# Kernel optimization log

Hardware: AMD Instinct MI355X
Metric: run time of the kernel (lower is better)

## Reference

```python
import jax, jax.numpy as jnp
import numpy as np

N_CLASS = 29   # len('SE?abcdefghijklmnopqrstuvwxyz')
N_HIDDEN = 128


def _rnn(x, h0, Wih, Whh, bih, bhh):
    """PyTorch nn.RNN (tanh, 1 layer, batch_first) semantics.
    x: [B,T,I], h0: [B,H]. Returns (outputs [B,T,H], h_T [B,H]).
    h_t = tanh(x_t @ Wih^T + bih + h_{t-1} @ Whh^T + bhh)
    """
    # Precompute input projection for all timesteps (batched GEMM).
    xp = jnp.einsum('bti,hi->bth', x, Wih) + (bih + bhh)  # [B,T,H]

    def step(h, xt):  # xt: [B,H]
        h_new = jnp.tanh(xt + h @ Whh.T)
        return h_new, h_new

    hT, hs = jax.lax.scan(step, h0, jnp.swapaxes(xp, 0, 1))  # scan over T
    return jnp.swapaxes(hs, 0, 1), hT


def setup_inputs() -> dict:
    key = jax.random.key(0)
    ks = jax.random.split(key, 12)
    B, T = 2048, 256
    s = 1.0 / np.sqrt(N_HIDDEN)  # PyTorch RNN/Linear init scale
    inp = {
        'encoder_input': jax.random.normal(ks[0], (B, T, N_CLASS), jnp.float32),
        'encoder_hidden': jnp.zeros((1, B, N_HIDDEN), jnp.float32),
        'decoder_input': jax.random.normal(ks[1], (B, T, N_CLASS), jnp.float32),
        'enc_Wih': jax.random.uniform(ks[2], (N_HIDDEN, N_CLASS), jnp.float32, -s, s),
        'enc_Whh': jax.random.uniform(ks[3], (N_HIDDEN, N_HIDDEN), jnp.float32, -s, s),
        'enc_bih': jax.random.uniform(ks[4], (N_HIDDEN,), jnp.float32, -s, s),
        'enc_bhh': jax.random.uniform(ks[5], (N_HIDDEN,), jnp.float32, -s, s),
        'dec_Wih': jax.random.uniform(ks[6], (N_HIDDEN, N_CLASS), jnp.float32, -s, s),
        'dec_Whh': jax.random.uniform(ks[7], (N_HIDDEN, N_HIDDEN), jnp.float32, -s, s),
        'dec_bih': jax.random.uniform(ks[8], (N_HIDDEN,), jnp.float32, -s, s),
        'dec_bhh': jax.random.uniform(ks[9], (N_HIDDEN,), jnp.float32, -s, s),
        'fc_W': jax.random.uniform(ks[10], (N_CLASS, N_HIDDEN), jnp.float32, -s, s),
        'fc_b': jax.random.uniform(ks[11], (N_CLASS,), jnp.float32, -s, s),
    }
    return inp


def reference(encoder_input, encoder_hidden, decoder_input,
              enc_Wih, enc_Whh, enc_bih, enc_bhh,
              dec_Wih, dec_Whh, dec_bih, dec_bhh,
              fc_W, fc_b):
    h0 = encoder_hidden[0]                                   # [B,H]
    _, h_t = _rnn(encoder_input, h0, enc_Wih, enc_Whh, enc_bih, enc_bhh)
    dec_out, _ = _rnn(decoder_input, h_t, dec_Wih, dec_Whh, dec_bih, dec_bhh)  # [B,T,H]
    return jnp.einsum('bth,ch->btc', dec_out, fc_W) + fc_b   # [B,T,n_class]
```

## Files before the change

kernel.cpp:

```cpp
#include <hip/hip_runtime.h>
#include <math.h>

#define TT 256
#define NI 29
#define HH 128
#define NC 29
#define ROWS 16
#define PSTR 136

typedef _Float16 f16x8 __attribute__((ext_vector_type(8)));
typedef _Float16 f16x4 __attribute__((ext_vector_type(4)));
typedef float f32x4 __attribute__((ext_vector_type(4)));

__device__ __forceinline__ float fast_tanh(float x) {
    float e = __builtin_amdgcn_exp2f(x * 2.885390081777927f);
    return 1.0f - 2.0f * __builtin_amdgcn_rcpf(e + 1.0f);
}

__device__ __forceinline__ f16x8 cvt8(const float4& a, const float4& b) {
    f16x8 r;
    r[0] = (_Float16)a.x; r[1] = (_Float16)a.y;
    r[2] = (_Float16)a.z; r[3] = (_Float16)a.w;
    r[4] = (_Float16)b.x; r[5] = (_Float16)b.y;
    r[6] = (_Float16)b.z; r[7] = (_Float16)b.w;
    return r;
}

__device__ __forceinline__ f16x4 tanh4(const f32x4& a) {
    f16x4 r;
#pragma unroll
    for (int q = 0; q < 4; ++q) r[q] = (_Float16)fast_tanh(a[q]);
    return r;
}

__device__ __forceinline__ f16x8 pack44(const f16x4& a, const f16x4& b) {
    f16x8 r;
    r[0] = a[0]; r[1] = a[1]; r[2] = a[2]; r[3] = a[3];
    r[4] = b[0]; r[5] = b[1]; r[6] = b[2]; r[7] = b[3];
    return r;
}

__device__ __forceinline__ void load_xe(const float* p, int g, float4& a, float4& b) {
    a = *(const float4*)p;
    if (g < 3) {
        b = *(const float4*)(p + 4);
    } else {
        b.x = p[4];
        b.y = 1.0f;
        b.z = 0.f; b.w = 0.f;
    }
}

#define MFMA16(A, B, C) __builtin_amdgcn_mfma_f32_16x16x32_f16((A), (B), (C), 0, 0, 0)

__device__ __forceinline__ void load_rnn_W(
    const float* __restrict__ Wih, const float* __restrict__ Whh,
    const float* __restrict__ bih, const float* __restrict__ bhh,
    int w, int m, int g, f16x8 (&AwO)[2][4], f16x8 (&AXO)[2])
{
#pragma unroll
    for (int a = 0; a < 2; ++a) {
        const int j = 32 * w + 4 * a + 8 * (m >> 2) + (m & 3);
#pragma unroll
        for (int k = 0; k < 4; ++k) {
            const int s = (w + k) & 3;
            const float* p = Whh + j * HH + 32 * s + 8 * g;
            AwO[a][k] = cvt8(*(const float4*)p, *(const float4*)(p + 4));
        }
        f16x8 ax;
#pragma unroll
        for (int e = 0; e < 8; ++e) {
            int kk = 8 * g + e;
            float v = (kk < NI) ? Wih[j * NI + kk]
                                : (kk == NI ? bih[j] + bhh[j] : 0.f);
            ax[e] = (_Float16)v;
        }
        AXO[a] = ax;
    }
}

#define STEP(CUR, XA, XB, TV, DECF)                                           \
  {                                                                           \
    f16x8 BX = cvt8(XA, XB);                                                  \
    f16x8 cb0 = own, cb1 = rd0, cb2 = rd1, cb3 = rd2;                         \
    f32x4 p00 = MFMA16(AXO[0], BX, zc);                                       \
    f32x4 p10 = MFMA16(AXO[1], BX, zc);                                       \
    p00 = MFMA16(AwO[0][0], cb0, p00);                                        \
    p10 = MFMA16(AwO[1][0], cb0, p10);                                        \
    f32x4 p01 = MFMA16(AwO[0][1], cb1, zc);                                   \
    f32x4 p11 = MFMA16(AwO[1][1], cb1, zc);                                   \
    p00 = MFMA16(AwO[0][2], cb2, p00);                                        \
    p10 = MFMA16(AwO[1][2], cb2, p10);                                        \
    p01 = MFMA16(AwO[0][3], cb3, p01);                                        \
    p11 = MFMA16(AwO[1][3], cb3, p11);                                        \
    if ((TV) + 2 < TT) load_xe(xrow + ((TV) + 2) * NI, g, XA, XB);            \
    f32x4 ac0 = p00 + p01, ac1 = p10 + p11;                                   \
    f16x4 t0 = tanh4(ac0), t1 = tanh4(ac1);                                   \
    own = pack44(t0, t1);                                                     \
    *(f16x8*)&planes[(CUR) ^ 1][m][wr_off] = own;                             \
    asm volatile("s_waitcnt lgkmcnt(0)" ::: "memory");                        \
    __builtin_amdgcn_s_barrier();                                             \
    __builtin_amdgcn_sched_barrier(0);                                        \
    rd0 = *(const f16x8*)&planes[(CUR) ^ 1][m][rb1];                          \
    rd1 = *(const f16x8*)&planes[(CUR) ^ 1][m][rb2];                          \
    rd2 = *(const f16x8*)&planes[(CUR) ^ 1][m][rb3];                          \
    if ((DECF) && w >= 2 && (TV) > 0) {                                       \
      f32x4 f0 = MFMA16(AfcO[0], cb0, zc);                                    \
      f0 = MFMA16(AfcO[1], cb1, f0);                                          \
      f0 = MFMA16(AfcO[2], cb2, f0);                                          \
      f0 = MFMA16(AfcO[3], cb3, f0);                                          \
      float* op = outp + (long)((TV) - 1) * NC + cbase;                       \
      _Pragma("unroll") for (int q = 0; q < 4; ++q)                           \
        if (cbase + q < NC) op[q] = f0[q] + fcbv[q];                          \
    }                                                                         \
  }

__launch_bounds__(256, 1)
__global__ void seq2seq_fused(const float* __restrict__ enc_in,
                              const float* __restrict__ h0p,
                              const float* __restrict__ dec_in,
                              const float* __restrict__ eWih,
                              const float* __restrict__ eWhh,
                              const float* __restrict__ ebih,
                              const float* __restrict__ ebhh,
                              const float* __restrict__ dWih,
                              const float* __restrict__ dWhh,
                              const float* __restrict__ dbih,
                              const float* __restrict__ dbhh,
                              const float* __restrict__ fcW,
                              const float* __restrict__ fcb,
                              float* __restrict__ out)
{
    __shared__ __align__(16) _Float16 planes[2][ROWS][PSTR];

    const int tid  = threadIdx.x;
    const int w    = tid >> 6;
    const int lane = tid & 63;
    const int m    = lane & 15;
    const int g    = lane >> 4;
    const int b0   = blockIdx.x * ROWS;

    const int wr_off = 32 * w + 8 * g;
    const int rb1 = 32 * ((w + 1) & 3) + 8 * g;
    const int rb2 = 32 * ((w + 2) & 3) + 8 * g;
    const int rb3 = 32 * ((w + 3) & 3) + 8 * g;

    const f32x4 zc = {0.f, 0.f, 0.f, 0.f};

    f16x8 AwO[2][4], AXO[2], AfcO[4];
    float fcbv[4] = {};
    f16x8 own, rd0, rd1, rd2;

    load_rnn_W(eWih, eWhh, ebih, ebhh, w, m, g, AwO, AXO);

    {
        const float* hp = h0p + (long)(b0 + m) * HH + wr_off;
        own = cvt8(*(const float4*)hp, *(const float4*)(hp + 4));
        *(f16x8*)&planes[0][m][wr_off] = own;
    }
    __syncthreads();
    rd0 = *(const f16x8*)&planes[0][m][rb1];
    rd1 = *(const f16x8*)&planes[0][m][rb2];
    rd2 = *(const f16x8*)&planes[0][m][rb3];

    const float* xrow = enc_in + (long)(b0 + m) * TT * NI + 8 * g;
    float* outp = out + (long)(b0 + m) * TT * NC;
    int cbase = 0;

    float4 xa0, xa1, xb0, xb1;
    load_xe(xrow, g, xa0, xa1);
    load_xe(xrow + NI, g, xb0, xb1);

    for (int t = 0; t < TT; t += 2) {
        STEP(0, xa0, xa1, t, 0);
        STEP(1, xb0, xb1, t + 1, 0);
    }

    load_rnn_W(dWih, dWhh, dbih, dbhh, w, m, g, AwO, AXO);
    if (w >= 2) {
        const int ct = w - 2;
        cbase = 16 * ct + 4 * g;
        const int c = 16 * ct + m;
#pragma unroll
        for (int k = 0; k < 4; ++k) {
            const int s = (w + k) & 3;
            f16x8 a;
#pragma unroll
            for (int e = 0; e < 8; ++e) {
                int kk = 32 * s + 8 * g + e;
                a[e] = (c < NC) ? (_Float16)fcW[c * HH + kk] : (_Float16)0.f;
            }
            AfcO[k] = a;
        }
#pragma unroll
        for (int q = 0; q < 4; ++q) {
            int c2 = cbase + q;
            fcbv[q] = (c2 < NC) ? fcb[c2] : 0.f;
        }
    }
    xrow = dec_in + (long)(b0 + m) * TT * NI + 8 * g;
    load_xe(xrow, g, xa0, xa1);
    load_xe(xrow + NI, g, xb0, xb1);

    for (int t = 0; t < TT; t += 2) {
        STEP(0, xa0, xa1, t, 1);
        STEP(1, xb0, xb1, t + 1, 1);
    }

    if (w >= 2) {
        f32x4 f0 = MFMA16(AfcO[0], own, zc);
        f0 = MFMA16(AfcO[1], rd0, f0);
        f0 = MFMA16(AfcO[2], rd1, f0);
        f0 = MFMA16(AfcO[3], rd2, f0);
        float* op = outp + (long)(TT - 1) * NC + cbase;
#pragma unroll
        for (int q = 0; q < 4; ++q)
            if (cbase + q < NC) op[q] = f0[q] + fcbv[q];
    }
}

extern "C" void kernel_launch(void* const* d_in, const int* in_sizes, int n_in,
                              void* d_out, int out_size, void* d_ws, size_t ws_size,
                              hipStream_t stream) {
    const float* enc_in  = (const float*)d_in[0];
    const float* enc_h0  = (const float*)d_in[1];
    const float* dec_in  = (const float*)d_in[2];
    const float* enc_Wih = (const float*)d_in[3];
    const float* enc_Whh = (const float*)d_in[4];
    const float* enc_bih = (const float*)d_in[5];
    const float* enc_bhh = (const float*)d_in[6];
    const float* dec_Wih = (const float*)d_in[7];
    const float* dec_Whh = (const float*)d_in[8];
    const float* dec_bih = (const float*)d_in[9];
    const float* dec_bhh = (const float*)d_in[10];
    const float* fc_W    = (const float*)d_in[11];
    const float* fc_b    = (const float*)d_in[12];
    float* out = (float*)d_out;

    dim3 grid(2048 / ROWS), block(256);
    seq2seq_fused<<<grid, block, 0, stream>>>(enc_in, enc_h0, dec_in,
                                              enc_Wih, enc_Whh, enc_bih, enc_bhh,
                                              dec_Wih, dec_Whh, dec_bih, dec_bhh,
                                              fc_W, fc_b, out);
}
```

Measured before the change: 465.8 us.

## Split decoder input projection and FC head into separate parallel kernels

Adds a pre-pass kernel that computes the decoder input projection for all timesteps into an fp16 workspace, and a post-pass kernel that applies the FC layer to decoder hidden states stored in that workspace. The recurrent kernel's decoder loop now only does the Whh MFMAs and tanh, overwriting the projection slot with the new hidden state. The per-step MFMA chain is also restructured into a single accumulator chain, with LDS reads moved to the start of each step. This shortens the serial critical path but adds about 128MB of workspace traffic and two extra launches, and the fast path depends on the workspace being large enough.

```diff
diff --git a/kernel.cpp b/kernel.cpp
--- a/kernel.cpp
+++ b/kernel.cpp
@@ -7,6 +7,9 @@
 #define NC 29
 #define ROWS 16
 #define PSTR 136
+#define BB 2048L
+#define BT (BB * TT)
+#define WS_NEED (BT * HH * 2)
 
 typedef _Float16 f16x8 __attribute__((ext_vector_type(8)));
 typedef _Float16 f16x4 __attribute__((ext_vector_type(4)));
@@ -40,14 +43,21 @@
     return r;
 }
 
+__device__ __forceinline__ void load_x0(const float* p, int g, float4& a, float4& b) {
+    a = *(const float4*)p;
+    if (g < 3) {
+        b = *(const float4*)(p + 4);
+    } else {
+        b.x = p[4]; b.y = 0.f; b.z = 0.f; b.w = 0.f;
+    }
+}
+
 __device__ __forceinline__ void load_xe(const float* p, int g, float4& a, float4& b) {
     a = *(const float4*)p;
     if (g < 3) {
         b = *(const float4*)(p + 4);
     } else {
-        b.x = p[4];
-        b.y = 1.0f;
-        b.z = 0.f; b.w = 0.f;
+        b.x = p[4]; b.y = 1.0f; b.z = 0.f; b.w = 0.f;
     }
 }
 
@@ -79,44 +89,151 @@
     }
 }
 
-#define STEP(CUR, XA, XB, TV, DECF)                                           \
+__launch_bounds__(256)
+__global__ void xp_kernel(const float* __restrict__ x,
+                          const float* __restrict__ Wih,
+                          const float* __restrict__ bih,
+                          const float* __restrict__ bhh,
+                          _Float16* __restrict__ xp)
+{
+    const int tid  = threadIdx.x;
+    const int lane = tid & 63;
+    const int wv   = tid >> 6;
+    const int m    = lane & 15;
+    const int g    = lane >> 4;
+    const long bt0 = ((long)blockIdx.x * 4 + wv) * 16;
+
+    f16x8 A[8];
+#pragma unroll
+    for (int jt = 0; jt < 8; ++jt) {
+        float4 v0, v1;
+        load_x0(Wih + (16 * jt + m) * NI + 8 * g, g, v0, v1);
+        A[jt] = cvt8(v0, v1);
+    }
+    float4 u0, u1;
+    load_x0(x + (bt0 + m) * NI + 8 * g, g, u0, u1);
+    f16x8 Bx = cvt8(u0, u1);
+
+    const f32x4 z = {0.f, 0.f, 0.f, 0.f};
+    f32x4 acc[8];
+#pragma unroll
+    for (int jt = 0; jt < 8; ++jt)
+        acc[jt] = MFMA16(A[jt], Bx, z);
+
+#pragma unroll
+    for (int jt = 0; jt < 8; ++jt) {
+        f16x4 o;
+#pragma unroll
+        for (int q = 0; q < 4; ++q) {
+            int j = 16 * jt + 4 * g + q;
+            o[q] = (_Float16)(acc[jt][q] + bih[j] + bhh[j]);
+        }
+        *(f16x4*)(xp + (bt0 + m) * HH + 16 * jt + 4 * g) = o;
+    }
+}
+
+__launch_bounds__(256)
+__global__ void fc_kernel(const _Float16* __restrict__ hws,
+                          const float* __restrict__ fcW,
+                          const float* __restrict__ fcb,
+                          float* __restrict__ out)
+{
+    const int tid  = threadIdx.x;
+    const int lane = tid & 63;
+    const int wv   = tid >> 6;
+    const int m    = lane & 15;
+    const int g    = lane >> 4;
+    const long bt0 = ((long)blockIdx.x * 4 + wv) * 16;
+
+    f16x8 A0[4], A1[4];
+#pragma unroll
+    for (int s = 0; s < 4; ++s) {
+        f16x8 a0, a1;
+        const int c1 = 16 + m;
+#pragma unroll
+        for (int e = 0; e < 8; ++e) {
+            int k = 32 * s + 8 * g + e;
+            a0[e] = (_Float16)fcW[m * HH + k];
+            a1[e] = (c1 < NC) ? (_Float16)fcW[c1 * HH + k] : (_Float16)0.f;
+        }
+        A0[s] = a0; A1[s] = a1;
+    }
+    f16x8 Bh[4];
+#pragma unroll
+    for (int s = 0; s < 4; ++s)
+        Bh[s] = *(const f16x8*)(hws + (bt0 + m) * HH + 32 * s + 8 * g);
+
+    const f32x4 z = {0.f, 0.f, 0.f, 0.f};
+    f32x4 f0 = MFMA16(A0[0], Bh[0], z);
+    f32x4 f1 = MFMA16(A1[0], Bh[0], z);
+    f0 = MFMA16(A0[1], Bh[1], f0);
+    f1 = MFMA16(A1[1], Bh[1], f1);
+    f0 = MFMA16(A0[2], Bh[2], f0);
+    f1 = MFMA16(A1[2], Bh[2], f1);
+    f0 = MFMA16(A0[3], Bh[3], f0);
+    f1 = MFMA16(A1[3], Bh[3], f1);
+
+    float* op = out + (bt0 + m) * NC;
+#pragma unroll
+    for (int q = 0; q < 4; ++q) {
+        op[4 * g + q] = f0[q] + fcb[4 * g + q];
+        int c = 16 + 4 * g + q;
+        if (c < NC) op[c] = f1[q] + fcb[c];
+    }
+}
+
+#define STEPE(CUR, XA, XB, TV, DECF)                                          \
   {                                                                           \
+    f16x8 rd0 = *(const f16x8*)&planes[CUR][m][rb1];                          \
+    f16x8 rd1 = *(const f16x8*)&planes[CUR][m][rb2];                          \
+    f16x8 rd2 = *(const f16x8*)&planes[CUR][m][rb3];                          \
     f16x8 BX = cvt8(XA, XB);                                                  \
-    f16x8 cb0 = own, cb1 = rd0, cb2 = rd1, cb3 = rd2;                         \
-    f32x4 p00 = MFMA16(AXO[0], BX, zc);                                       \
-    f32x4 p10 = MFMA16(AXO[1], BX, zc);                                       \
-    p00 = MFMA16(AwO[0][0], cb0, p00);                                        \
-    p10 = MFMA16(AwO[1][0], cb0, p10);                                        \
-    f32x4 p01 = MFMA16(AwO[0][1], cb1, zc);                                   \
-    f32x4 p11 = MFMA16(AwO[1][1], cb1, zc);                                   \
-    p00 = MFMA16(AwO[0][2], cb2, p00);                                        \
-    p10 = MFMA16(AwO[1][2], cb2, p10);                                        \
-    p01 = MFMA16(AwO[0][3], cb3, p01);                                        \
-    p11 = MFMA16(AwO[1][3], cb3, p11);                                        \
     if ((TV) + 2 < TT) load_xe(xrow + ((TV) + 2) * NI, g, XA, XB);            \
-    f32x4 ac0 = p00 + p01, ac1 = p10 + p11;                                   \
-    f16x4 t0 = tanh4(ac0), t1 = tanh4(ac1);                                   \
-    own = pack44(t0, t1);                                                     \
+    f32x4 ac0 = MFMA16(AXO[0], BX, zc);                                       \
+    f32x4 ac1 = MFMA16(AXO[1], BX, zc);                                       \
+    ac0 = MFMA16(AwO[0][0], own, ac0);  ac1 = MFMA16(AwO[1][0], own, ac1);    \
+    ac0 = MFMA16(AwO[0][1], rd0, ac0);  ac1 = MFMA16(AwO[1][1], rd0, ac1);    \
+    ac0 = MFMA16(AwO[0][2], rd1, ac0);  ac1 = MFMA16(AwO[1][2], rd1, ac1);    \
+    ac0 = MFMA16(AwO[0][3], rd2, ac0);  ac1 = MFMA16(AwO[1][3], rd2, ac1);    \
+    if ((DECF) && w >= 2 && (TV) > 0) {                                       \
+      f32x4 f0 = MFMA16(AfcO[0], own, zc);                                    \
+      f0 = MFMA16(AfcO[1], rd0, f0);                                          \
+      f0 = MFMA16(AfcO[2], rd1, f0);                                          \
+      f0 = MFMA16(AfcO[3], rd2, f0);                                          \
+      float* op = outp + (long)((TV) - 1) * NC + cbase;                       \
+      _Pragma("unroll") for (int q = 0; q < 4; ++q)                           \
+        if (cbase + q < NC) op[q] = f0[q] + fcbv[q];                          \
+    }                                                                         \
+    own = pack44(tanh4(ac0), tanh4(ac1));                                     \
     *(f16x8*)&planes[(CUR) ^ 1][m][wr_off] = own;                             \
     asm volatile("s_waitcnt lgkmcnt(0)" ::: "memory");                        \
     __builtin_amdgcn_s_barrier();                                             \
     __builtin_amdgcn_sched_barrier(0);                                        \
-    rd0 = *(const f16x8*)&planes[(CUR) ^ 1][m][rb1];                          \
-    rd1 = *(const f16x8*)&planes[(CUR) ^ 1][m][rb2];                          \
-    rd2 = *(const f16x8*)&planes[(CUR) ^ 1][m][rb3];                          \
-    if ((DECF) && w >= 2 && (TV) > 0) {                                       \
-      f32x4 f0 = MFMA16(AfcO[0], cb0, zc);                                    \
-      f0 = MFMA16(AfcO[1], cb1, f0);                                          \
-      f0 = MFMA16(AfcO[2], cb2, f0);                                          \
-      f0 = MFMA16(AfcO[3], cb3, f0);                                          \
-      float* op = outp + (long)((TV) - 1) * NC + cbase;                       \
-      _Pragma("unroll") for (int q = 0; q < 4; ++q)                           \
-        if (cbase + q < NC) op[q] = f0[q] + fcbv[q];                          \
-    }                                                                         \
   }
 
+#define STEPD(CUR, XQ, TV)                                                    \
+  {                                                                           \
+    f16x8 rd0 = *(const f16x8*)&planes[CUR][m][rb1];                          \
+    f16x8 rd1 = *(const f16x8*)&planes[CUR][m][rb2];                          \
+    f16x8 rd2 = *(const f16x8*)&planes[CUR][m][rb3];                          \
+    f32x4 ac0 = {(float)XQ[0], (float)XQ[1], (float)XQ[2], (float)XQ[3]};     \
+    f32x4 ac1 = {(float)XQ[4], (float)XQ[5], (float)XQ[6], (float)XQ[7]};     \
+    if ((TV) + 4 < TT) XQ = *(const f16x8*)(xh + ((TV) + 4) * HH);            \
+    ac0 = MFMA16(AwO[0][0], own, ac0);  ac1 = MFMA16(AwO[1][0], own, ac1);    \
+    ac0 = MFMA16(AwO[0][1], rd0, ac0);  ac1 = MFMA16(AwO[1][1], rd0, ac1);    \
+    ac0 = MFMA16(AwO[0][2], rd1, ac0);  ac1 = MFMA16(AwO[1][2], rd1, ac1);    \
+    ac0 = MFMA16(AwO[0][3], rd2, ac0);  ac1 = MFMA16(AwO[1][3], rd2, ac1);    \
+    own = pack44(tanh4(ac0), tanh4(ac1));                                     \
+    *(f16x8*)(xh + (long)(TV) * HH) = own;                                    \
+    *(f16x8*)&planes[(CUR) ^ 1][m][wr_off] = own;                             \
+    asm volatile("s_waitcnt lgkmcnt(0)" ::: "memory");                        \
+    __builtin_amdgcn_s_barrier();                                             \
+    __builtin_amdgcn_sched_barrier(0);                                        \
+  }
+
+template <int XP>
 __launch_bounds__(256, 1)
-__global__ void seq2seq_fused(const float* __restrict__ enc_in,
+__global__ void seq2seq_chain(const float* __restrict__ enc_in,
                               const float* __restrict__ h0p,
                               const float* __restrict__ dec_in,
                               const float* __restrict__ eWih,
@@ -129,6 +246,7 @@
                               const float* __restrict__ dbhh,
                               const float* __restrict__ fcW,
                               const float* __restrict__ fcb,
+                              _Float16* __restrict__ hws,
                               float* __restrict__ out)
 {
     __shared__ __align__(16) _Float16 planes[2][ROWS][PSTR];
@@ -149,73 +267,87 @@
 
     f16x8 AwO[2][4], AXO[2], AfcO[4];
     float fcbv[4] = {};
-    f16x8 own, rd0, rd1, rd2;
+    int cbase = 0;
+    f16x8 own;
 
     load_rnn_W(eWih, eWhh, ebih, ebhh, w, m, g, AwO, AXO);
-
     {
         const float* hp = h0p + (long)(b0 + m) * HH + wr_off;
         own = cvt8(*(const float4*)hp, *(const float4*)(hp + 4));
         *(f16x8*)&planes[0][m][wr_off] = own;
     }
     __syncthreads();
-    rd0 = *(const f16x8*)&planes[0][m][rb1];
-    rd1 = *(const f16x8*)&planes[0][m][rb2];
-    rd2 = *(const f16x8*)&planes[0][m][rb3];
 
     const float* xrow = enc_in + (long)(b0 + m) * TT * NI + 8 * g;
     float* outp = out + (long)(b0 + m) * TT * NC;
-    int cbase = 0;
-
-    float4 xa0, xa1, xb0, xb1;
-    load_xe(xrow, g, xa0, xa1);
-    load_xe(xrow + NI, g, xb0, xb1);
-
-    for (int t = 0; t < TT; t += 2) {
-        STEP(0, xa0, xa1, t, 0);
-        STEP(1, xb0, xb1, t + 1, 0);
+
+    {
+        float4 xa0, xa1, xb0, xb1;
+        load_xe(xrow, g, xa0, xa1);
+        load_xe(xrow + NI, g, xb0, xb1);
+        for (int t = 0; t < TT; t += 2) {
+            STEPE(0, xa0, xa1, t, 0);
+            STEPE(1, xb0, xb1, t + 1, 0);
+        }
     }
 
     load_rnn_W(dWih, dWhh, dbih, dbhh, w, m, g, AwO, AXO);
-    if (w >= 2) {
-        const int ct = w - 2;
-        cbase = 16 * ct + 4 * g;
-        const int c = 16 * ct + m;
-#pragma unroll
-        for (int k = 0; k < 4; ++k) {
-            const int s = (w + k) & 3;
-            f16x8 a;
-#pragma unroll
-            for (int e = 0; e < 8; ++e) {
-                int kk = 32 * s + 8 * g + e;
-                a[e] = (c < NC) ? (_Float16)fcW[c * HH + kk] : (_Float16)0.f;
+
+    if (XP) {
+        _Float16* xh = hws + (long)(b0 + m) * TT * HH + wr_off;
+        f16x8 xq0 = *(const f16x8*)(xh + 0 * HH);
+        f16x8 xq1 = *(const f16x8*)(xh + 1 * HH);
+        f16x8 xq2 = *(const f16x8*)(xh + 2 * HH);
+        f16x8 xq3 = *(const f16x8*)(xh + 3 * HH);
+        for (int t = 0; t < TT; t += 4) {
+            STEPD(0, xq0, t);
+            STEPD(1, xq1, t + 1);
+            STEPD(0, xq2, t + 2);
+            STEPD(1, xq3, t + 3);
+        }
+    } else {
+        if (w >= 2) {
+            const int ct = w - 2;
+            cbase = 16 * ct + 4 * g;
+            const int c = 16 * ct + m;
+#pragma unroll
+            for (int k = 0; k < 4; ++k) {
+                const int s = (w + k) & 3;
+                f16x8 a;
+#pragma unroll
+                for (int e = 0; e < 8; ++e) {
+                    int kk = 32 * s + 8 * g + e;
+                    a[e] = (c < NC) ? (_Float16)fcW[c * HH + kk] : (_Float16)0.f;
+                }
+                AfcO[k] = a;
             }
-            AfcO[k] = a;
-        }
-#pragma unroll
-        for (int q = 0; q < 4; ++q) {
-            int c2 = cbase + q;
-            fcbv[q] = (c2 < NC) ? fcb[c2] : 0.f;
-        }
-    }
-    xrow = dec_in + (long)(b0 + m) * TT * NI + 8 * g;
-    load_xe(xrow, g, xa0, xa1);
-    load_xe(xrow + NI, g, xb0, xb1);
-
-    for (int t = 0; t < TT; t += 2) {
-        STEP(0, xa0, xa1, t, 1);
-        STEP(1, xb0, xb1, t + 1, 1);
-    }
-
-    if (w >= 2) {
-        f32x4 f0 = MFMA16(AfcO[0], own, zc);
-        f0 = MFMA16(AfcO[1], rd0, f0);
-        f0 = MFMA16(AfcO[2], rd1, f0);
-        f0 = MFMA16(AfcO[3], rd2, f0);
-        float* op = outp + (long)(TT - 1) * NC + cbase;
-#pragma unroll
-        for (int q = 0; q < 4; ++q)
-            if (cbase + q < NC) op[q] = f0[q] + fcbv[q];
+#pragma unroll
+            for (int q = 0; q < 4; ++q) {
+                int c2 = cbase + q;
+                fcbv[q] = (c2 < NC) ? fcb[c2] : 0.f;
+            }
+        }
+        xrow = dec_in + (long)(b0 + m) * TT * NI + 8 * g;
+        float4 xa0, xa1, xb0, xb1;
+        load_xe(xrow, g, xa0, xa1);
+        load_xe(xrow + NI, g, xb0, xb1);
+        for (int t = 0; t < TT; t += 2) {
+            STEPE(0, xa0, xa1, t, 1);
+            STEPE(1, xb0, xb1, t + 1, 1);
+        }
+        if (w >= 2) {
+            f16x8 rd0 = *(const f16x8*)&planes[0][m][rb1];
+            f16x8 rd1 = *(const f16x8*)&planes[0][m][rb2];
+            f16x8 rd2 = *(const f16x8*)&planes[0][m][rb3];
+            f32x4 f0 = MFMA16(AfcO[0], own, zc);
+            f0 = MFMA16(AfcO[1], rd0, f0);
+            f0 = MFMA16(AfcO[2], rd1, f0);
+            f0 = MFMA16(AfcO[3], rd2, f0);
+            float* op = outp + (long)(TT - 1) * NC + cbase;
+#pragma unroll
+            for (int q = 0; q < 4; ++q)
+                if (cbase + q < NC) op[q] = f0[q] + fcbv[q];
+        }
     }
 }
 
@@ -237,9 +369,22 @@
     const float* fc_b    = (const float*)d_in[12];
     float* out = (float*)d_out;
 
-    dim3 grid(2048 / ROWS), block(256);
-    seq2seq_fused<<<grid, block, 0, stream>>>(enc_in, enc_h0, dec_in,
-                                              enc_Wih, enc_Whh, enc_bih, enc_bhh,
-                                              dec_Wih, dec_Whh, dec_bih, dec_bhh,
-                                              fc_W, fc_b, out);
-}
+    dim3 grid(BB / ROWS), block(256);
+    const bool fast = (ws_size >= (size_t)WS_NEED);
+
+    if (fast) {
+        _Float16* hws = (_Float16*)d_ws;
+        dim3 xgrid((unsigned)(BT / 64)), xblock(256);
+        xp_kernel<<<xgrid, xblock, 0, stream>>>(dec_in, dec_Wih, dec_bih, dec_bhh, hws);
+        seq2seq_chain<1><<<grid, block, 0, stream>>>(enc_in, enc_h0, dec_in,
+                                                     enc_Wih, enc_Whh, enc_bih, enc_bhh,
+                                                     dec_Wih, dec_Whh, dec_bih, dec_bhh,
+                                                     fc_W, fc_b, hws, out);
+        fc_kernel<<<xgrid, xblock, 0, stream>>>(hws, fc_W, fc_b, out);
+    } else {
+        seq2seq_chain<0><<<grid, block, 0, stream>>>(enc_in, enc_h0, dec_in,
+                                                     enc_Wih, enc_Whh, enc_bih, enc_bhh,
+                                                     dec_Wih, dec_Whh, dec_bih, dec_bhh,
+                                                     fc_W, fc_b, nullptr, out);
+    }
+}
```

New measurement: 675.1 us. +44.9%, slower.
